# Kernel tuning notes

Measured on AMD Instinct MI355X. Metric: run time of the kernel, lower is better.

The kernel has to match this reference:

```python
import jax, jax.numpy as jnp
import numpy as np

M, B, E, A = 3, 65536, 512, 256  # modalities, batch, embedding_dim, attention_dim
LN_EPS = 1e-5


def setup_inputs() -> dict:
    key = jax.random.key(0)
    ks = jax.random.split(key, 9)
    s_e = 1.0 / np.sqrt(E)
    s_a = 1.0 / np.sqrt(A)
    return {
        "x": jax.random.normal(ks[0], (M, B, E), jnp.float32),
        "Wq": jax.random.normal(ks[1], (M, E, A), jnp.float32) * s_e,
        "bq": jax.random.normal(ks[2], (M, A), jnp.float32) * s_e,
        "Wk": jax.random.normal(ks[3], (M, E, A), jnp.float32) * s_e,
        "bk": jax.random.normal(ks[4], (M, A), jnp.float32) * s_e,
        "v": jax.random.normal(ks[5], (M, A), jnp.float32) * s_a,
        "Wt": jax.random.normal(ks[6], (M, M, E, E), jnp.float32) * s_e,
        "bt": jax.random.normal(ks[7], (M, M, E), jnp.float32) * s_e,
        "gamma": jnp.ones((M * E,), jnp.float32),
        "beta": jnp.zeros((M * E,), jnp.float32),
    }


def reference(x, Wq, bq, Wk, bk, v, Wt, bt, gamma, beta):
    # Per-modality query/key projections (batched over modality axis m).
    qp = jnp.einsum('mbe,mea->mba', x, Wq) + bq[:, None, :]  # [M,B,A]
    kp = jnp.einsum('mbe,mea->mba', x, Wk) + bk[:, None, :]  # [M,B,A]
    # Additive score: v_q^T tanh(q_proj[q] + k_proj[k]) for every (q,k) pair.
    t = jnp.tanh(qp[:, None, :, :] + kp[None, :, :, :])       # [Q,K,B,A]
    scores = jnp.einsum('qa,qkba->qkb', v, t)                  # [Q,K,B]
    # Exclude k == q from the softmax (torch code skips key_mod == query_mod).
    diag = jnp.eye(scores.shape[0], dtype=bool)[:, :, None]
    scores = jnp.where(diag, -jnp.inf, scores)
    alpha = jax.nn.softmax(scores, axis=1)                     # [Q,K,B], zero on diag
    # Weighted sum of per-pair linear transforms of the key embeddings.
    att = (jnp.einsum('qkb,kbe,qkef->qbf', alpha, x, Wt)
           + jnp.einsum('qkb,qke->qbe', alpha, bt))            # [Q,B,E]
    attended = x + att                                         # residual per modality
    # Concat modalities along features, then LayerNorm over M*E.
    fused = jnp.transpose(attended, (1, 0, 2)).reshape(x.shape[1], -1)  # [B, M*E]
    mu = jnp.mean(fused, axis=-1, keepdims=True)
    var = jnp.var(fused, axis=-1, keepdims=True)
    fused = (fused - mu) * jax.lax.rsqrt(var + LN_EPS) * gamma + beta
    return fused
```

## Files before the change

kernel.cpp:

```cpp
#include <hip/hip_runtime.h>
#include <hip/hip_bf16.h>

#define MOD   3
#define BATCH 65536
#define EDIM  512
#define ADIM  256
#define FEAT  1536

typedef __attribute__((ext_vector_type(8))) short   s16x8;
typedef __attribute__((ext_vector_type(8))) __bf16  bf16x8;
typedef __attribute__((ext_vector_type(4))) float   f32x4;
typedef __attribute__((ext_vector_type(4))) unsigned short u16x4;

__device__ __forceinline__ float b2f(unsigned short u) {
    union { unsigned int ui; float f; } c; c.ui = ((unsigned int)u) << 16; return c.f;
}
__device__ __forceinline__ unsigned short f2b(float f) {
    __hip_bfloat16 h = __float2bfloat16(f);
    return __builtin_bit_cast(unsigned short, h);
}

__device__ __forceinline__ void glds16(const unsigned short* g, unsigned short* l) {
    __builtin_amdgcn_global_load_lds(
        (const __attribute__((address_space(1))) void*)g,
        (__attribute__((address_space(3))) void*)l, 16, 0, 0);
}

#define WAITV(N) asm volatile("s_waitcnt vmcnt(%0)" :: "i"(N) : "memory")
__device__ __forceinline__ void BAR() {
    asm volatile("" ::: "memory");
    __builtin_amdgcn_s_barrier();
    asm volatile("" ::: "memory");
}

__global__ __launch_bounds__(256) void k_convert_x(const float* __restrict__ x,
                                                   unsigned short* __restrict__ xb, int n4) {
    int i = blockIdx.x * blockDim.x + threadIdx.x;
    int stride = gridDim.x * blockDim.x;
    for (; i < n4; i += stride) {
        f32x4 v = *((const f32x4*)x + i);
        u16x4 o;
        for (int j = 0; j < 4; ++j) o[j] = f2b(v[j]);
        *((u16x4*)xb + i) = o;
    }
}

__global__ __launch_bounds__(256) void k_prep_w(const float* __restrict__ Wq,
                                                const float* __restrict__ Wk,
                                                const float* __restrict__ Wt,
                                                unsigned short* __restrict__ wqk,
                                                unsigned short* __restrict__ wtt2) {
    int i = blockIdx.x * blockDim.x + threadIdx.x;
    int stride = gridDim.x * blockDim.x;
    for (int idx = i; idx < MOD * EDIM * EDIM; idx += stride) {
        int m = idx / (EDIM * EDIM); int r = idx % (EDIM * EDIM);
        int n = r / EDIM; int e = r % EDIM;
        float f = (n < ADIM) ? Wq[(m * EDIM + e) * ADIM + n]
                             : Wk[(m * EDIM + e) * ADIM + (n - ADIM)];
        wqk[idx] = f2b(f);
    }
    for (int idx = i; idx < MOD * 1024 * EDIM; idx += stride) {
        int k = idx / (1024 * EDIM); int r = idx % (1024 * EDIM);
        int n = r / EDIM; int e = r % EDIM;
        int q = (n < EDIM) ? (k + 1) % 3 : (k + 2) % 3;
        int f = (n < EDIM) ? n : n - EDIM;
        wtt2[idx] = f2b(Wt[((size_t)(q * 3 + k) * EDIM + e) * EDIM + f]);
    }
}


struct GCtx {
    const unsigned short* pA;
    const unsigned short* pB;
    const unsigned short* lds;
    unsigned short* ldsW;
    int aoff, boff;
};

__device__ __forceinline__ void stage_s(const GCtx& c, int s) {
    if (s >= 32) return;
    int colK = (s >> 2) * 64 + (s & 2) * 16;
    const unsigned short* src = ((s & 1) ? c.pB : c.pA) + colK;
    unsigned short* dst = c.ldsW + (s & 7) * 8192;
    glds16(src, dst);
    glds16(src + 16 * 512, dst + 512);
}

template<int Q>
__device__ __forceinline__ void phase_compute(int T, const GCtx& c,
                                              s16x8 (&bfr)[4], f32x4 (&acc)[8][4]) {
    constexpr int ks = Q >> 1, rh = Q & 1;
    const unsigned short* Asl = c.lds + ((T & 1) * 4 + 2 * ks) * 8192;
    const unsigned short* Bsl = Asl + 8192;
    s16x8 af[4];
#pragma unroll
    for (int i = 0; i < 4; ++i) af[i] = *(const s16x8*)(Asl + c.aoff + (rh * 4 + i) * 512);
    if constexpr ((Q & 1) == 0) {
#pragma unroll
        for (int j = 0; j < 4; ++j) bfr[j] = *(const s16x8*)(Bsl + c.boff + j * 512);
    }
    __builtin_amdgcn_s_setprio(1);
#pragma unroll
    for (int i = 0; i < 4; ++i)
#pragma unroll
        for (int j = 0; j < 4; ++j)
            acc[rh * 4 + i][j] = __builtin_amdgcn_mfma_f32_16x16x32_bf16(
                __builtin_bit_cast(bf16x8, af[i]), __builtin_bit_cast(bf16x8, bfr[j]),
                acc[rh * 4 + i][j], 0, 0, 0);
    __builtin_amdgcn_s_setprio(0);
}

template<int W0, int W2>
__device__ __forceinline__ void do_tile(int T, const GCtx& c,
                                        s16x8 (&bfr)[4], f32x4 (&acc)[8][4]) {
    stage_s(c, 4 * T + 6);
    WAITV(W0); BAR();
    phase_compute<0>(T, c, bfr, acc);
    BAR();
    stage_s(c, 4 * T + 7);
    phase_compute<1>(T, c, bfr, acc);
    BAR();
    stage_s(c, 4 * T + 8);
    WAITV(W2); BAR();
    phase_compute<2>(T, c, bfr, acc);
    BAR();
    stage_s(c, 4 * T + 9);
    phase_compute<3>(T, c, bfr, acc);
    BAR();
}

__device__ __forceinline__ void gemm256_core(const unsigned short* Ag,
                                             const unsigned short* Bg,
                                             unsigned short* lds, f32x4 (&acc)[8][4]) {
    const int tid = threadIdx.x, lane = tid & 63, wid = tid >> 6;
    const int wm = wid >> 2, wn = wid & 3;
    GCtx c;
    int stageRow = wid * 32 + (lane >> 2);
    int gsrc8 = ((lane & 3) ^ ((lane >> 3) & 3)) * 8;
    c.pA = Ag + (size_t)stageRow * 512 + gsrc8;
    c.pB = Bg + (size_t)stageRow * 512 + gsrc8;
    c.lds = lds;
    c.ldsW = lds + wid * 1024;
    int swz8 = ((lane >> 4) ^ ((lane >> 1) & 3)) * 8;
    c.aoff = (wm * 128 + (lane & 15)) * 32 + swz8;
    c.boff = (wn * 64 + (lane & 15)) * 32 + swz8;
    s16x8 bfr[4];
#pragma unroll
    for (int s = 0; s < 6; ++s) stage_s(c, s);
#pragma unroll 1
    for (int t = 0; t < 6; ++t) do_tile<10, 10>(t, c, bfr, acc);
    do_tile<10, 8>(6, c, bfr, acc);
    do_tile<4, 0>(7, c, bfr, acc);
}

__global__ __launch_bounds__(512, 2) void k_gemm_proj(const unsigned short* __restrict__ xb,
                                                      const unsigned short* __restrict__ wqk,
                                                      const float* __restrict__ bq,
                                                      const float* __restrict__ bk,
                                                      unsigned short* __restrict__ proj) {
    __shared__ __align__(16) unsigned short LDS[65536];
    int l = (blockIdx.x & 7) * 192 + (blockIdx.x >> 3);
    int ct = l & 1, rt = (l >> 1) & 255, m = l >> 9;
    int row0 = rt * 256, col0 = ct * 256;
    f32x4 acc[8][4];
#pragma unroll
    for (int i = 0; i < 8; ++i) for (int j = 0; j < 4; ++j) acc[i][j] = (f32x4)0.f;
    gemm256_core(xb + ((size_t)m * BATCH + row0) * EDIM,
                 wqk + ((size_t)m * EDIM + col0) * EDIM, LDS, acc);
    int lane = threadIdx.x & 63, wid = threadIdx.x >> 6;
    int wm = wid >> 2, wn = wid & 3;
#pragma unroll
    for (int j = 0; j < 4; ++j) {
        int col = col0 + wn * 64 + j * 16 + (lane & 15);
        float bias = (col < ADIM) ? bq[m * ADIM + col] : bk[m * ADIM + col - ADIM];
#pragma unroll
        for (int i8 = 0; i8 < 8; ++i8) {
            int rbase = row0 + wm * 128 + i8 * 16 + (lane >> 4) * 4;
#pragma unroll
            for (int r = 0; r < 4; ++r)
                proj[((size_t)m * BATCH + rbase + r) * EDIM + col] = f2b(acc[i8][j][r] + bias);
        }
    }
}

__global__ __launch_bounds__(256) void k_scores(const unsigned short* __restrict__ proj,
                                                const float* __restrict__ v,
                                                float* __restrict__ alpha) {
    int wid = threadIdx.x >> 6, lane = threadIdx.x & 63;
    size_t b = (size_t)blockIdx.x * 4 + wid;
    float qp[3][4], kp[3][4], vq[3][4];
    for (int m = 0; m < 3; ++m) {
        const unsigned short* p = proj + ((size_t)m * BATCH + b) * EDIM;
        u16x4 uq = *(const u16x4*)(p + lane * 4);
        u16x4 uk = *(const u16x4*)(p + ADIM + lane * 4);
        f32x4 vv = *((const f32x4*)(v + m * ADIM) + lane);
        for (int j = 0; j < 4; ++j) { qp[m][j] = b2f(uq[j]); kp[m][j] = b2f(uk[j]); vq[m][j] = vv[j]; }
    }
    for (int q = 0; q < 3; ++q) {
        float s[2];
        for (int ki = 0; ki < 2; ++ki) {
            int k = (q + 1 + ki) % 3;
            float a = 0.f;
            for (int j = 0; j < 4; ++j) a += vq[q][j] * tanhf(qp[q][j] + kp[k][j]);
            for (int off = 32; off; off >>= 1) a += __shfl_xor(a, off, 64);
            s[ki] = a;
        }
        if (lane == 0) {
            float mx = fmaxf(s[0], s[1]);
            float e0 = expf(s[0] - mx), e1 = expf(s[1] - mx);
            float inv = 1.f / (e0 + e1);
            alpha[(size_t)(q * 2 + 0) * BATCH + b] = e0 * inv;
            alpha[(size_t)(q * 2 + 1) * BATCH + b] = e1 * inv;
        }
    }
}

__global__ __launch_bounds__(512, 2) void k_gemm_y(const unsigned short* __restrict__ xb,
                                                   const unsigned short* __restrict__ wtt2,
                                                   unsigned short* __restrict__ y) {
    __shared__ __align__(16) unsigned short LDS[65536];
    int l = (blockIdx.x & 7) * 384 + (blockIdx.x >> 3);
    int ct = l & 3, rt = (l >> 2) & 255, k = l >> 10;
    int row0 = rt * 256, col0 = ct * 256;
    f32x4 acc[8][4];
#pragma unroll
    for (int i = 0; i < 8; ++i) for (int j = 0; j < 4; ++j) acc[i][j] = (f32x4)0.f;
    gemm256_core(xb + ((size_t)k * BATCH + row0) * EDIM,
                 wtt2 + ((size_t)k * 1024 + col0) * EDIM, LDS, acc);
    int lane = threadIdx.x & 63, wid = threadIdx.x >> 6;
    int wm = wid >> 2, wn = wid & 3;
    int p  = (ct < 2) ? (((k + 1) % 3) * 2 + 1) : (((k + 2) % 3) * 2 + 0);
    int cb = (ct < 2) ? col0 : (col0 - EDIM);
#pragma unroll
    for (int j = 0; j < 4; ++j) {
        int col = cb + wn * 64 + j * 16 + (lane & 15);
#pragma unroll
        for (int i8 = 0; i8 < 8; ++i8) {
            int rbase = row0 + wm * 128 + i8 * 16 + (lane >> 4) * 4;
#pragma unroll
            for (int r = 0; r < 4; ++r)
                y[((size_t)p * BATCH + rbase + r) * EDIM + col] = f2b(acc[i8][j][r]);
        }
    }
}

__global__ __launch_bounds__(192) void k_fuse_ln(const unsigned short* __restrict__ xb,
                                                 const unsigned short* __restrict__ y,
                                                 const float* __restrict__ alpha,
                                                 const float* __restrict__ bt,
                                                 const float* __restrict__ gamma,
                                                 const float* __restrict__ beta,
                                                 float* __restrict__ out) {
    __shared__ float red[2][3];
    int b = blockIdx.x, t = threadIdx.x, m = t >> 6, lane = t & 63;
    int e0 = lane * 8;
    float a0 = alpha[(size_t)(m * 2 + 0) * BATCH + b];
    float a1 = alpha[(size_t)(m * 2 + 1) * BATCH + b];
    s16x8 xv = *(const s16x8*)(xb + ((size_t)m * BATCH + b) * EDIM + e0);
    s16x8 y0 = *(const s16x8*)(y + ((size_t)(m * 2 + 0) * BATCH + b) * EDIM + e0);
    s16x8 y1 = *(const s16x8*)(y + ((size_t)(m * 2 + 1) * BATCH + b) * EDIM + e0);
    int kA = (m + 1) % 3, kB = (m + 2) % 3;
    const float* bA = bt + (size_t)(m * 3 + kA) * EDIM + e0;
    const float* bB = bt + (size_t)(m * 3 + kB) * EDIM + e0;
    f32x4 bA0 = *(const f32x4*)bA, bA1 = *(const f32x4*)(bA + 4);
    f32x4 bB0 = *(const f32x4*)bB, bB1 = *(const f32x4*)(bB + 4);
    float v[8]; float s = 0.f, s2 = 0.f;
#pragma unroll
    for (int j = 0; j < 8; ++j) {
        float ba = (j < 4) ? bA0[j] : bA1[j - 4];
        float bb = (j < 4) ? bB0[j] : bB1[j - 4];
        float vv = b2f((unsigned short)xv[j]) + a0 * (b2f((unsigned short)y0[j]) + ba)
                                             + a1 * (b2f((unsigned short)y1[j]) + bb);
        v[j] = vv; s += vv; s2 += vv * vv;
    }
    for (int off = 32; off; off >>= 1) { s += __shfl_xor(s, off, 64); s2 += __shfl_xor(s2, off, 64); }
    if (lane == 0) { red[0][m] = s; red[1][m] = s2; }
    __syncthreads();
    float S = red[0][0] + red[0][1] + red[0][2];
    float S2 = red[1][0] + red[1][1] + red[1][2];
    float mu  = S * (1.f / 1536.f);
    float var = S2 * (1.f / 1536.f) - mu * mu;
    float rs  = rsqrtf(var + 1e-5f);
    int f0 = m * EDIM + e0;
    f32x4 g0 = *(const f32x4*)(gamma + f0), g1 = *(const f32x4*)(gamma + f0 + 4);
    f32x4 be0 = *(const f32x4*)(beta + f0), be1 = *(const f32x4*)(beta + f0 + 4);
    f32x4 o0, o1;
#pragma unroll
    for (int j = 0; j < 4; ++j) {
        o0[j] = (v[j]     - mu) * rs * g0[j] + be0[j];
        o1[j] = (v[j + 4] - mu) * rs * g1[j] + be1[j];
    }
    float* op = out + (size_t)b * FEAT + f0;
    *(f32x4*)op = o0; *(f32x4*)(op + 4) = o1;
}

extern "C" void kernel_launch(void* const* d_in, const int* in_sizes, int n_in,
                              void* d_out, int out_size, void* d_ws, size_t ws_size,
                              hipStream_t stream) {
    const float* x     = (const float*)d_in[0];
    const float* Wq    = (const float*)d_in[1];
    const float* bq    = (const float*)d_in[2];
    const float* Wk    = (const float*)d_in[3];
    const float* bk    = (const float*)d_in[4];
    const float* v     = (const float*)d_in[5];
    const float* Wt    = (const float*)d_in[6];
    const float* bt    = (const float*)d_in[7];
    const float* gamma = (const float*)d_in[8];
    const float* beta  = (const float*)d_in[9];
    float* out = (float*)d_out;

    char* ws = (char*)d_ws;
    unsigned short* wqk   = (unsigned short*)(ws);
    unsigned short* wtt2  = (unsigned short*)(ws + 1572864);
    float*          alpha = (float*)        (ws + 4718592);
    unsigned short* xb    = (unsigned short*)(ws + 6291456);
    unsigned short* y     = (unsigned short*)(ws + 207618048);
    unsigned short* proj  = y;

    k_convert_x<<<4096, 256, 0, stream>>>(x, xb, (MOD * BATCH * EDIM) / 4);
    k_prep_w   <<<2048, 256, 0, stream>>>(Wq, Wk, Wt, wqk, wtt2);
    k_gemm_proj<<<1536, 512, 0, stream>>>(xb, wqk, bq, bk, proj);
    k_scores   <<<16384, 256, 0, stream>>>(proj, v, alpha);
    k_gemm_y   <<<3072, 512, 0, stream>>>(xb, wtt2, y);
    k_fuse_ln  <<<65536, 192, 0, stream>>>(xb, y, alpha, bt, gamma, beta, out);
}
```

Baseline: 899.7 us.

## Fuse alpha-weighted sum of both key transforms into one K=1024 GEMM

```diff
diff --git a/kernel.cpp b/kernel.cpp
--- a/kernel.cpp
+++ b/kernel.cpp
@@ -49,7 +49,7 @@
                                                 const float* __restrict__ Wk,
                                                 const float* __restrict__ Wt,
                                                 unsigned short* __restrict__ wqk,
-                                                unsigned short* __restrict__ wtt2) {
+                                                unsigned short* __restrict__ wtt3) {
     int i = blockIdx.x * blockDim.x + threadIdx.x;
     int stride = gridDim.x * blockDim.x;
     for (int idx = i; idx < MOD * EDIM * EDIM; idx += stride) {
@@ -60,27 +60,48 @@
         wqk[idx] = f2b(f);
     }
     for (int idx = i; idx < MOD * 1024 * EDIM; idx += stride) {
-        int k = idx / (1024 * EDIM); int r = idx % (1024 * EDIM);
+        int q = idx / (1024 * EDIM); int r = idx % (1024 * EDIM);
         int n = r / EDIM; int e = r % EDIM;
-        int q = (n < EDIM) ? (k + 1) % 3 : (k + 2) % 3;
-        int f = (n < EDIM) ? n : n - EDIM;
-        wtt2[idx] = f2b(Wt[((size_t)(q * 3 + k) * EDIM + e) * EDIM + f]);
+        int kp = n >> 9, f = n & 511;
+        int k = (q + 1 + kp) % 3;
+        wtt3[idx] = f2b(Wt[((size_t)(q * 3 + k) * EDIM + e) * EDIM + f]);
     }
 }
 
 
 struct GCtx {
-    const unsigned short* pA;
-    const unsigned short* pB;
+    const unsigned short* pA[2];
+    const unsigned short* pB[2];
     const unsigned short* lds;
     unsigned short* ldsW;
     int aoff, boff;
 };
 
+__device__ __forceinline__ void gctx_init(GCtx& c,
+                                          const unsigned short* Ag0, const unsigned short* Ag1,
+                                          const unsigned short* Bg0, const unsigned short* Bg1,
+                                          unsigned short* lds) {
+    const int tid = threadIdx.x, lane = tid & 63, wid = tid >> 6;
+    const int wm = wid >> 2, wn = wid & 3;
+    int stageRow = wid * 32 + (lane >> 2);
+    int gsrc8 = ((lane & 3) ^ ((lane >> 3) & 3)) * 8;
+    size_t so = (size_t)stageRow * 512 + gsrc8;
+    c.pA[0] = Ag0 + so; c.pA[1] = Ag1 + so;
+    c.pB[0] = Bg0 + so; c.pB[1] = Bg1 + so;
+    c.lds = lds;
+    c.ldsW = lds + wid * 1024;
+    int swz8 = ((lane >> 4) ^ ((lane >> 1) & 3)) * 8;
+    c.aoff = (wm * 128 + (lane & 15)) * 32 + swz8;
+    c.boff = (wn * 64 + (lane & 15)) * 32 + swz8;
+}
+
+template<int NU>
 __device__ __forceinline__ void stage_s(const GCtx& c, int s) {
-    if (s >= 32) return;
-    int colK = (s >> 2) * 64 + (s & 2) * 16;
-    const unsigned short* src = ((s & 1) ? c.pB : c.pA) + colK;
+    if (s >= NU) return;
+    int p = s >> 5;
+    int sp = s & 31;
+    int colK = (sp >> 2) * 64 + (sp & 2) * 16;
+    const unsigned short* src = ((sp & 1) ? c.pB[p] : c.pA[p]) + colK;
     unsigned short* dst = c.ldsW + (s & 7) * 8192;
     glds16(src, dst);
     glds16(src + 16 * 512, dst + 512);
@@ -110,47 +131,23 @@
     __builtin_amdgcn_s_setprio(0);
 }
 
-template<int W0, int W2>
+template<int W0, int W2, int NU>
 __device__ __forceinline__ void do_tile(int T, const GCtx& c,
                                         s16x8 (&bfr)[4], f32x4 (&acc)[8][4]) {
-    stage_s(c, 4 * T + 6);
+    stage_s<NU>(c, 4 * T + 6);
     WAITV(W0); BAR();
     phase_compute<0>(T, c, bfr, acc);
     BAR();
-    stage_s(c, 4 * T + 7);
+    stage_s<NU>(c, 4 * T + 7);
     phase_compute<1>(T, c, bfr, acc);
     BAR();
-    stage_s(c, 4 * T + 8);
+    stage_s<NU>(c, 4 * T + 8);
     WAITV(W2); BAR();
     phase_compute<2>(T, c, bfr, acc);
     BAR();
-    stage_s(c, 4 * T + 9);
+    stage_s<NU>(c, 4 * T + 9);
     phase_compute<3>(T, c, bfr, acc);
     BAR();
-}
-
-__device__ __forceinline__ void gemm256_core(const unsigned short* Ag,
-                                             const unsigned short* Bg,
-                                             unsigned short* lds, f32x4 (&acc)[8][4]) {
-    const int tid = threadIdx.x, lane = tid & 63, wid = tid >> 6;
-    const int wm = wid >> 2, wn = wid & 3;
-    GCtx c;
-    int stageRow = wid * 32 + (lane >> 2);
-    int gsrc8 = ((lane & 3) ^ ((lane >> 3) & 3)) * 8;
-    c.pA = Ag + (size_t)stageRow * 512 + gsrc8;
-    c.pB = Bg + (size_t)stageRow * 512 + gsrc8;
-    c.lds = lds;
-    c.ldsW = lds + wid * 1024;
-    int swz8 = ((lane >> 4) ^ ((lane >> 1) & 3)) * 8;
-    c.aoff = (wm * 128 + (lane & 15)) * 32 + swz8;
-    c.boff = (wn * 64 + (lane & 15)) * 32 + swz8;
-    s16x8 bfr[4];
-#pragma unroll
-    for (int s = 0; s < 6; ++s) stage_s(c, s);
-#pragma unroll 1
-    for (int t = 0; t < 6; ++t) do_tile<10, 10>(t, c, bfr, acc);
-    do_tile<10, 8>(6, c, bfr, acc);
-    do_tile<4, 0>(7, c, bfr, acc);
 }
 
 __global__ __launch_bounds__(512, 2) void k_gemm_proj(const unsigned short* __restrict__ xb,
@@ -165,8 +162,17 @@
     f32x4 acc[8][4];
 #pragma unroll
     for (int i = 0; i < 8; ++i) for (int j = 0; j < 4; ++j) acc[i][j] = (f32x4)0.f;
-    gemm256_core(xb + ((size_t)m * BATCH + row0) * EDIM,
-                 wqk + ((size_t)m * EDIM + col0) * EDIM, LDS, acc);
+    GCtx c;
+    const unsigned short* Ag = xb + ((size_t)m * BATCH + row0) * EDIM;
+    const unsigned short* Bg = wqk + ((size_t)m * EDIM + col0) * EDIM;
+    gctx_init(c, Ag, Ag, Bg, Bg, LDS);
+    s16x8 bfr[4];
+#pragma unroll
+    for (int s = 0; s < 6; ++s) stage_s<32>(c, s);
+#pragma unroll 1
+    for (int t = 0; t < 6; ++t) do_tile<10, 10, 32>(t, c, bfr, acc);
+    do_tile<10, 8, 32>(6, c, bfr, acc);
+    do_tile<4, 0, 32>(7, c, bfr, acc);
     int lane = threadIdx.x & 63, wid = threadIdx.x >> 6;
     int wm = wid >> 2, wn = wid & 3;
 #pragma unroll
@@ -215,62 +221,95 @@
     }
 }
 
-__global__ __launch_bounds__(512, 2) void k_gemm_y(const unsigned short* __restrict__ xb,
-                                                   const unsigned short* __restrict__ wtt2,
-                                                   unsigned short* __restrict__ y) {
+__global__ __launch_bounds__(512, 2) void k_gemm_att(const unsigned short* __restrict__ xb,
+                                                     const unsigned short* __restrict__ wtt3,
+                                                     const float* __restrict__ alpha,
+                                                     const float* __restrict__ bt,
+                                                     unsigned short* __restrict__ att) {
     __shared__ __align__(16) unsigned short LDS[65536];
-    int l = (blockIdx.x & 7) * 384 + (blockIdx.x >> 3);
-    int ct = l & 3, rt = (l >> 2) & 255, k = l >> 10;
+    __shared__ float auxA0[256], auxA1[256], auxR[256];
+    int l = (blockIdx.x & 7) * 192 + (blockIdx.x >> 3);
+    int ct = l & 1, rt = (l >> 1) & 255, q = l >> 9;
     int row0 = rt * 256, col0 = ct * 256;
+    int kA = (q + 1) % 3, kB = (q + 2) % 3;
+    int tid = threadIdx.x, lane = tid & 63, wid = tid >> 6;
+    int wm = wid >> 2, wn = wid & 3;
+
+    if (tid < 256) {
+        float a0 = alpha[(size_t)(q * 2 + 0) * BATCH + row0 + tid];
+        float a1 = alpha[(size_t)(q * 2 + 1) * BATCH + row0 + tid];
+        auxA0[tid] = a0; auxA1[tid] = a1;
+        auxR[tid] = a0 / fmaxf(a1, 1e-30f);
+    }
+    __syncthreads();
+
     f32x4 acc[8][4];
 #pragma unroll
     for (int i = 0; i < 8; ++i) for (int j = 0; j < 4; ++j) acc[i][j] = (f32x4)0.f;
-    gemm256_core(xb + ((size_t)k * BATCH + row0) * EDIM,
-                 wtt2 + ((size_t)k * 1024 + col0) * EDIM, LDS, acc);
-    int lane = threadIdx.x & 63, wid = threadIdx.x >> 6;
-    int wm = wid >> 2, wn = wid & 3;
-    int p  = (ct < 2) ? (((k + 1) % 3) * 2 + 1) : (((k + 2) % 3) * 2 + 0);
-    int cb = (ct < 2) ? col0 : (col0 - EDIM);
+    GCtx c;
+    gctx_init(c,
+              xb + ((size_t)kA * BATCH + row0) * EDIM,
+              xb + ((size_t)kB * BATCH + row0) * EDIM,
+              wtt3 + ((size_t)(q * 2 + 0) * EDIM + col0) * EDIM,
+              wtt3 + ((size_t)(q * 2 + 1) * EDIM + col0) * EDIM,
+              LDS);
+    s16x8 bfr[4];
+#pragma unroll
+    for (int s = 0; s < 6; ++s) stage_s<64>(c, s);
+#pragma unroll 1
+    for (int t = 0; t < 8; ++t) do_tile<10, 10, 64>(t, c, bfr, acc);
+#pragma unroll
+    for (int i8 = 0; i8 < 8; ++i8) {
+        int rl = wm * 128 + i8 * 16 + (lane >> 4) * 4;
+        f32x4 rv = *(const f32x4*)&auxR[rl];
+#pragma unroll
+        for (int j = 0; j < 4; ++j)
+#pragma unroll
+            for (int r = 0; r < 4; ++r) acc[i8][j][r] *= rv[r];
+    }
+#pragma unroll 1
+    for (int t = 8; t < 14; ++t) do_tile<10, 10, 64>(t, c, bfr, acc);
+    do_tile<10, 8, 64>(14, c, bfr, acc);
+    do_tile<4, 0, 64>(15, c, bfr, acc);
+
+    float btAv[4], btBv[4];
 #pragma unroll
     for (int j = 0; j < 4; ++j) {
-        int col = cb + wn * 64 + j * 16 + (lane & 15);
-#pragma unroll
-        for (int i8 = 0; i8 < 8; ++i8) {
-            int rbase = row0 + wm * 128 + i8 * 16 + (lane >> 4) * 4;
+        int col = col0 + wn * 64 + j * 16 + (lane & 15);
+        btAv[j] = bt[(size_t)(q * 3 + kA) * EDIM + col];
+        btBv[j] = bt[(size_t)(q * 3 + kB) * EDIM + col];
+    }
+#pragma unroll
+    for (int i8 = 0; i8 < 8; ++i8) {
+        int rl = wm * 128 + i8 * 16 + (lane >> 4) * 4;
+        f32x4 a0v = *(const f32x4*)&auxA0[rl];
+        f32x4 a1v = *(const f32x4*)&auxA1[rl];
+        int rbase = row0 + rl;
+#pragma unroll
+        for (int j = 0; j < 4; ++j) {
+            int col = col0 + wn * 64 + j * 16 + (lane & 15);
 #pragma unroll
             for (int r = 0; r < 4; ++r)
-                y[((size_t)p * BATCH + rbase + r) * EDIM + col] = f2b(acc[i8][j][r]);
+                att[((size_t)q * BATCH + rbase + r) * EDIM + col] =
+                    f2b(a1v[r] * acc[i8][j][r] + a0v[r] * btAv[j] + a1v[r] * btBv[j]);
         }
     }
 }
 
 __global__ __launch_bounds__(192) void k_fuse_ln(const unsigned short* __restrict__ xb,
-                                                 const unsigned short* __restrict__ y,
-                                                 const float* __restrict__ alpha,
-                                                 const float* __restrict__ bt,
+                                                 const unsigned short* __restrict__ att,
                                                  const float* __restrict__ gamma,
                                                  const float* __restrict__ beta,
                                                  float* __restrict__ out) {
     __shared__ float red[2][3];
     int b = blockIdx.x, t = threadIdx.x, m = t >> 6, lane = t & 63;
     int e0 = lane * 8;
-    float a0 = alpha[(size_t)(m * 2 + 0) * BATCH + b];
-    float a1 = alpha[(size_t)(m * 2 + 1) * BATCH + b];
     s16x8 xv = *(const s16x8*)(xb + ((size_t)m * BATCH + b) * EDIM + e0);
-    s16x8 y0 = *(const s16x8*)(y + ((size_t)(m * 2 + 0) * BATCH + b) * EDIM + e0);
-    s16x8 y1 = *(const s16x8*)(y + ((size_t)(m * 2 + 1) * BATCH + b) * EDIM + e0);
-    int kA = (m + 1) % 3, kB = (m + 2) % 3;
-    const float* bA = bt + (size_t)(m * 3 + kA) * EDIM + e0;
-    const float* bB = bt + (size_t)(m * 3 + kB) * EDIM + e0;
-    f32x4 bA0 = *(const f32x4*)bA, bA1 = *(const f32x4*)(bA + 4);
-    f32x4 bB0 = *(const f32x4*)bB, bB1 = *(const f32x4*)(bB + 4);
+    s16x8 av = *(const s16x8*)(att + ((size_t)m * BATCH + b) * EDIM + e0);
     float v[8]; float s = 0.f, s2 = 0.f;
 #pragma unroll
     for (int j = 0; j < 8; ++j) {
-        float ba = (j < 4) ? bA0[j] : bA1[j - 4];
-        float bb = (j < 4) ? bB0[j] : bB1[j - 4];
-        float vv = b2f((unsigned short)xv[j]) + a0 * (b2f((unsigned short)y0[j]) + ba)
-                                             + a1 * (b2f((unsigned short)y1[j]) + bb);
+        float vv = b2f((unsigned short)xv[j]) + b2f((unsigned short)av[j]);
         v[j] = vv; s += vv; s2 += vv * vv;
     }
     for (int off = 32; off; off >>= 1) { s += __shfl_xor(s, off, 64); s2 += __shfl_xor(s2, off, 64); }
@@ -311,16 +350,16 @@
 
     char* ws = (char*)d_ws;
     unsigned short* wqk   = (unsigned short*)(ws);
-    unsigned short* wtt2  = (unsigned short*)(ws + 1572864);
+    unsigned short* wtt3  = (unsigned short*)(ws + 1572864);
     float*          alpha = (float*)        (ws + 4718592);
     unsigned short* xb    = (unsigned short*)(ws + 6291456);
-    unsigned short* y     = (unsigned short*)(ws + 207618048);
-    unsigned short* proj  = y;
+    unsigned short* att   = (unsigned short*)(ws + 207618048);
+    unsigned short* proj  = att;
 
     k_convert_x<<<4096, 256, 0, stream>>>(x, xb, (MOD * BATCH * EDIM) / 4);
-    k_prep_w   <<<2048, 256, 0, stream>>>(Wq, Wk, Wt, wqk, wtt2);
+    k_prep_w   <<<2048, 256, 0, stream>>>(Wq, Wk, Wt, wqk, wtt3);
     k_gemm_proj<<<1536, 512, 0, stream>>>(xb, wqk, bq, bk, proj);
     k_scores   <<<16384, 256, 0, stream>>>(proj, v, alpha);
-    k_gemm_y   <<<3072, 512, 0, stream>>>(xb, wtt2, y);
-    k_fuse_ln  <<<65536, 192, 0, stream>>>(xb, y, alpha, bt, gamma, beta, out);
-}
+    k_gemm_att <<<1536, 512, 0, stream>>>(xb, wtt3, alpha, bt, att);
+    k_fuse_ln  <<<65536, 192, 0, stream>>>(xb, att, gamma, beta, out);
+}
```

Measured after the change: 751.1 us. -16.5%, faster.
